# Performance work log

Measured on AMD Instinct MI355X. Metric: run time of the kernel, lower is better.

Reference implementation:

```python
import jax, jax.numpy as jnp
import numpy as np

N, C, T, V = 64, 64, 256, 25
R, O = C // 8, 64  # rel_channels, out_channels
ALPHA = 1.0


def setup_inputs() -> dict:
    key = jax.random.key(0)
    ks = jax.random.split(key, 10)
    s = 0.05
    return {
        "x": jax.random.normal(ks[0], (N, C, T, V), dtype=jnp.float32),
        "A": jax.random.normal(ks[1], (V, V), dtype=jnp.float32),
        "w1": jax.random.normal(ks[2], (R, C), dtype=jnp.float32) * s,
        "b1": jnp.zeros((R,), dtype=jnp.float32),
        "w2": jax.random.normal(ks[3], (R, C), dtype=jnp.float32) * s,
        "b2": jnp.zeros((R,), dtype=jnp.float32),
        "w3": jax.random.normal(ks[4], (O, C), dtype=jnp.float32) * s,
        "b3": jnp.zeros((O,), dtype=jnp.float32),
        "w4": jax.random.normal(ks[5], (O, R), dtype=jnp.float32) * s,
        "b4": jnp.zeros((O,), dtype=jnp.float32),
    }


def reference(x, A, w1, b1, w2, b2, w3, b3, w4, b4):
    # x: (N, C, T, V)
    # conv1/conv2 are 1x1 convs followed by mean over T -> (N, R, V)
    x1 = jnp.einsum('nctv,rc->nrv', x, w1) / x.shape[2] + b1[:, None]
    x2 = jnp.einsum('nctv,rc->nrv', x, w2) / x.shape[2] + b2[:, None]
    # conv3: 1x1 conv -> (N, O, T, V)
    x3 = jnp.einsum('nctv,oc->notv', x, w3) + b3[:, None, None]
    # outer-difference attention over joints: (N, R, V, V)
    att = jnp.tanh(x1[:, :, :, None] - x2[:, :, None, :])
    # conv4 channel mix (R->O), scale, add adjacency: (N, O, V, V)
    m = jnp.einsum('nruv,or->nouv', att, w4) + b4[:, None, None]
    m = m * ALPHA + A[None, None, :, :]
    # aggregation: einsum('ncuv,nctv->nctu')
    out = jnp.einsum('ncuv,nctv->nctu', m, x3)
    return out
```

## Files before the change

kernel.cpp:

```cpp
#include <hip/hip_runtime.h>

#define NN 64
#define CC 64
#define TT 256
#define VV 25
#define RR 8
#define OO 64
#define PLANE 6400

__global__ __launch_bounds__(256) void k_xsum(const float* __restrict__ x,
                                              float* __restrict__ xsum) {
  int nc = blockIdx.x;
  const float* src = x + (size_t)nc * PLANE;
  __shared__ float s[PLANE];
  int tid = threadIdx.x;
#pragma unroll
  for (int k = 0; k < 25; ++k) s[k * 256 + tid] = src[k * 256 + tid];
  __syncthreads();
  if (tid < VV) {
    float a0 = 0.f, a1 = 0.f, a2 = 0.f, a3 = 0.f;
    for (int t = 0; t < TT; t += 4) {
      a0 += s[(t + 0) * VV + tid];
      a1 += s[(t + 1) * VV + tid];
      a2 += s[(t + 2) * VV + tid];
      a3 += s[(t + 3) * VV + tid];
    }
    xsum[nc * VV + tid] = (a0 + a1) + (a2 + a3);
  }
}

__global__ void k_wt(const float* __restrict__ w3, float* __restrict__ w3t) {
  int k = blockIdx.x * 256 + threadIdx.x;
  if (k < 4096) {
    int c = k >> 6, o = k & 63;
    w3t[k] = w3[o * 64 + c];
  }
}

__global__ __launch_bounds__(256) void k_build_m(
    const float* __restrict__ xsum, const float* __restrict__ A,
    const float* __restrict__ w1, const float* __restrict__ b1,
    const float* __restrict__ w2, const float* __restrict__ b2,
    const float* __restrict__ w4, const float* __restrict__ b4,
    float* __restrict__ mp) {
  int n = blockIdx.x;
  __shared__ float xs[CC * VV];
  __shared__ float sx1[RR * VV];
  __shared__ float sx2[RR * VV];
  __shared__ float att[RR * 625];
  int tid = threadIdx.x;
  const float* xsn = xsum + n * (CC * VV);
  for (int k = tid; k < CC * VV; k += 256) xs[k] = xsn[k];
  __syncthreads();
  if (tid < RR * VV) {
    int r = tid / VV, v = tid % VV;
    float a1 = 0.f, a2 = 0.f;
#pragma unroll
    for (int c = 0; c < CC; ++c) {
      float xv = xs[c * VV + v];
      a1 = fmaf(w1[r * CC + c], xv, a1);
      a2 = fmaf(w2[r * CC + c], xv, a2);
    }
    sx1[tid] = a1 * (1.f / 256.f) + b1[r];
    sx2[tid] = a2 * (1.f / 256.f) + b2[r];
  }
  __syncthreads();
  for (int k = tid; k < RR * 625; k += 256) {
    int r = k / 625, uv = k % 625;
    int u = uv / VV, v = uv % VV;
    att[k] = tanhf(sx1[r * VV + u] - sx2[r * VV + v]);
  }
  __syncthreads();
  for (int k = tid; k < OO * 625; k += 256) {
    int o = k / 625, uv = k % 625;
    int u = uv / VV, v = uv % VV;
    float a = b4[o] + A[uv];
#pragma unroll
    for (int r = 0; r < RR; ++r) a = fmaf(w4[o * RR + r], att[r * 625 + uv], a);
    mp[(((size_t)n * OO + o) * VV + u) * 32 + v] = a;
  }
}

__global__ __launch_bounds__(256) void k_conv3(const float* __restrict__ x,
                                               const float* __restrict__ w3t,
                                               const float* __restrict__ b3,
                                               float* __restrict__ x3) {
  int n = blockIdx.y;
  int p = blockIdx.x * 256 + threadIdx.x;
  const float* xn = x + (size_t)n * CC * PLANE;
  float acc[OO];
#pragma unroll
  for (int o = 0; o < OO; ++o) acc[o] = b3[o];
#pragma unroll 2
  for (int c = 0; c < CC; ++c) {
    float xv = xn[(size_t)c * PLANE + p];
    const float* w = w3t + c * OO;
#pragma unroll
    for (int o = 0; o < OO; ++o) acc[o] = fmaf(w[o], xv, acc[o]);
  }
  float* dst = x3 + (size_t)n * OO * PLANE + p;
#pragma unroll
  for (int o = 0; o < OO; ++o) dst[(size_t)o * PLANE] = acc[o];
}

__global__ __launch_bounds__(256) void k_aggr(float* __restrict__ out,
                                              const float* __restrict__ mp) {
  int no = blockIdx.x;
  float* base = out + (size_t)no * PLANE;
  __shared__ float s[PLANE];
  int tid = threadIdx.x;
#pragma unroll
  for (int k = 0; k < 25; ++k) s[k * 256 + tid] = base[k * 256 + tid];
  __syncthreads();
  const float* m = mp + (size_t)no * (VV * 32);
  float xr[VV], orow[VV];
#pragma unroll
  for (int v = 0; v < VV; ++v) xr[v] = s[tid * VV + v];
#pragma unroll
  for (int u = 0; u < VV; ++u) {
    float a = 0.f;
#pragma unroll
    for (int v = 0; v < VV; ++v) a = fmaf(m[u * 32 + v], xr[v], a);
    orow[u] = a;
  }
#pragma unroll
  for (int u = 0; u < VV; ++u) s[tid * VV + u] = orow[u];
  __syncthreads();
#pragma unroll
  for (int k = 0; k < 25; ++k) base[k * 256 + tid] = s[k * 256 + tid];
}

extern "C" void kernel_launch(void* const* d_in, const int* in_sizes, int n_in,
                              void* d_out, int out_size, void* d_ws,
                              size_t ws_size, hipStream_t stream) {
  const float* x = (const float*)d_in[0];
  const float* A = (const float*)d_in[1];
  const float* w1 = (const float*)d_in[2];
  const float* b1 = (const float*)d_in[3];
  const float* w2 = (const float*)d_in[4];
  const float* b2 = (const float*)d_in[5];
  const float* w3 = (const float*)d_in[6];
  const float* b3 = (const float*)d_in[7];
  const float* w4 = (const float*)d_in[8];
  const float* b4 = (const float*)d_in[9];
  float* out = (float*)d_out;
  float* ws = (float*)d_ws;

  float* xsum = ws;
  float* w3t = ws + 102400;
  float* mp = ws + 106496;

  k_xsum<<<NN * CC, 256, 0, stream>>>(x, xsum);
  k_wt<<<16, 256, 0, stream>>>(w3, w3t);
  k_build_m<<<NN, 256, 0, stream>>>(xsum, A, w1, b1, w2, b2, w4, b4, mp);
  k_conv3<<<dim3(PLANE / 256, NN), 256, 0, stream>>>(x, w3t, b3, out);
  k_aggr<<<NN * OO, 256, 0, stream>>>(out, mp);
}
```

Before: 305.3 us.

## Fuse conv3 and aggregation into one kernel through shared memory

Merges the 1x1 conv3 and the joint aggregation into one kernel. Each block computes x3 for 8 time steps into shared memory, applies the transposed m matrix, and writes the output once, so the intermediate x3 no longer round-trips through global memory. Also folds the w3 transpose into k_xsum to drop a launch, and splits k_build_m over four output-channel groups for more parallelism, at the cost of each group recomputing att. Only 200 of 256 threads do the conv phase, and the aggregation phase keeps 50 accumulators per thread, which raises register pressure.

```diff
diff --git a/kernel.cpp b/kernel.cpp
--- a/kernel.cpp
+++ b/kernel.cpp
@@ -7,13 +7,21 @@
 #define RR 8
 #define OO 64
 #define PLANE 6400
+#define SX 226
 
 __global__ __launch_bounds__(256) void k_xsum(const float* __restrict__ x,
-                                              float* __restrict__ xsum) {
+                                              float* __restrict__ xsum,
+                                              const float* __restrict__ w3,
+                                              float* __restrict__ w3t) {
   int nc = blockIdx.x;
+  int tid = threadIdx.x;
+  if (blockIdx.x < 16) {
+    int k = blockIdx.x * 256 + tid;
+    int c = k >> 6, o = k & 63;
+    w3t[k] = w3[o * 64 + c];
+  }
   const float* src = x + (size_t)nc * PLANE;
   __shared__ float s[PLANE];
-  int tid = threadIdx.x;
 #pragma unroll
   for (int k = 0; k < 25; ++k) s[k * 256 + tid] = src[k * 256 + tid];
   __syncthreads();
@@ -29,14 +37,6 @@
   }
 }
 
-__global__ void k_wt(const float* __restrict__ w3, float* __restrict__ w3t) {
-  int k = blockIdx.x * 256 + threadIdx.x;
-  if (k < 4096) {
-    int c = k >> 6, o = k & 63;
-    w3t[k] = w3[o * 64 + c];
-  }
-}
-
 __global__ __launch_bounds__(256) void k_build_m(
     const float* __restrict__ xsum, const float* __restrict__ A,
     const float* __restrict__ w1, const float* __restrict__ b1,
@@ -44,6 +44,7 @@
     const float* __restrict__ w4, const float* __restrict__ b4,
     float* __restrict__ mp) {
   int n = blockIdx.x;
+  int og = blockIdx.y;
   __shared__ float xs[CC * VV];
   __shared__ float sx1[RR * VV];
   __shared__ float sx2[RR * VV];
@@ -71,63 +72,80 @@
     att[k] = tanhf(sx1[r * VV + u] - sx2[r * VV + v]);
   }
   __syncthreads();
-  for (int k = tid; k < OO * 625; k += 256) {
-    int o = k / 625, uv = k % 625;
-    int u = uv / VV, v = uv % VV;
-    float a = b4[o] + A[uv];
+  for (int k = tid; k < 16 * 625; k += 256) {
+    int o = og * 16 + k / 625, vu = k % 625;
+    int v = vu / VV, u = vu % VV;
+    float a = b4[o] + A[u * VV + v];
 #pragma unroll
-    for (int r = 0; r < RR; ++r) a = fmaf(w4[o * RR + r], att[r * 625 + uv], a);
-    mp[(((size_t)n * OO + o) * VV + u) * 32 + v] = a;
+    for (int r = 0; r < RR; ++r)
+      a = fmaf(w4[o * RR + r], att[r * 625 + u * VV + v], a);
+    mp[(((size_t)n * OO + o) * VV + v) * 32 + u] = a;
   }
 }
 
-__global__ __launch_bounds__(256) void k_conv3(const float* __restrict__ x,
-                                               const float* __restrict__ w3t,
-                                               const float* __restrict__ b3,
-                                               float* __restrict__ x3) {
+__global__ __launch_bounds__(256, 2) void k_fused(
+    const float* __restrict__ x, const float* __restrict__ w3t,
+    const float* __restrict__ b3, const float* __restrict__ mp,
+    float* __restrict__ out) {
   int n = blockIdx.y;
-  int p = blockIdx.x * 256 + threadIdx.x;
-  const float* xn = x + (size_t)n * CC * PLANE;
-  float acc[OO];
+  int t0 = blockIdx.x * 8;
+  __shared__ float s[OO * SX];
+  int tid = threadIdx.x;
+
+  if (tid < 200) {
+    const float* xp = x + (size_t)n * CC * PLANE + t0 * VV + tid;
+    float acc[OO];
 #pragma unroll
-  for (int o = 0; o < OO; ++o) acc[o] = b3[o];
+    for (int o = 0; o < OO; ++o) acc[o] = b3[o];
 #pragma unroll 2
-  for (int c = 0; c < CC; ++c) {
-    float xv = xn[(size_t)c * PLANE + p];
-    const float* w = w3t + c * OO;
+    for (int c = 0; c < CC; ++c) {
+      float xv = xp[(size_t)c * PLANE];
+      const float* w = w3t + c * OO;
 #pragma unroll
-    for (int o = 0; o < OO; ++o) acc[o] = fmaf(w[o], xv, acc[o]);
+      for (int o = 0; o < OO; ++o) acc[o] = fmaf(w[o], xv, acc[o]);
+    }
+#pragma unroll
+    for (int o = 0; o < OO; ++o) s[o * SX + tid] = acc[o];
   }
-  float* dst = x3 + (size_t)n * OO * PLANE + p;
+  __syncthreads();
+
+  {
+    int o = tid >> 2, tq = tid & 3;
+    const float* xA = s + o * SX + tq * VV;
+    const float* xB = xA + 4 * VV;
+    const float* mb = mp + (size_t)(n * OO + o) * VV * 32;
+    float accA[VV], accB[VV];
 #pragma unroll
-  for (int o = 0; o < OO; ++o) dst[(size_t)o * PLANE] = acc[o];
-}
+    for (int u = 0; u < VV; ++u) {
+      accA[u] = 0.f;
+      accB[u] = 0.f;
+    }
+#pragma unroll 2
+    for (int v = 0; v < VV; ++v) {
+      float xa = xA[v];
+      float xb = xB[v];
+      const float* mr = mb + v * 32;
+#pragma unroll
+      for (int u = 0; u < VV; ++u) {
+        float mv = mr[u];
+        accA[u] = fmaf(mv, xa, accA[u]);
+        accB[u] = fmaf(mv, xb, accB[u]);
+      }
+    }
+    __syncthreads();
+#pragma unroll
+    for (int u = 0; u < VV; ++u) {
+      s[o * SX + tq * VV + u] = accA[u];
+      s[o * SX + (tq + 4) * VV + u] = accB[u];
+    }
+  }
+  __syncthreads();
 
-__global__ __launch_bounds__(256) void k_aggr(float* __restrict__ out,
-                                              const float* __restrict__ mp) {
-  int no = blockIdx.x;
-  float* base = out + (size_t)no * PLANE;
-  __shared__ float s[PLANE];
-  int tid = threadIdx.x;
-#pragma unroll
-  for (int k = 0; k < 25; ++k) s[k * 256 + tid] = base[k * 256 + tid];
-  __syncthreads();
-  const float* m = mp + (size_t)no * (VV * 32);
-  float xr[VV], orow[VV];
-#pragma unroll
-  for (int v = 0; v < VV; ++v) xr[v] = s[tid * VV + v];
-#pragma unroll
-  for (int u = 0; u < VV; ++u) {
-    float a = 0.f;
-#pragma unroll
-    for (int v = 0; v < VV; ++v) a = fmaf(m[u * 32 + v], xr[v], a);
-    orow[u] = a;
+  float* ob = out + (size_t)n * OO * PLANE + t0 * VV;
+  for (int k = tid; k < OO * 200; k += 256) {
+    int oo = k / 200, p = k - oo * 200;
+    ob[(size_t)oo * PLANE + p] = s[oo * SX + p];
   }
-#pragma unroll
-  for (int u = 0; u < VV; ++u) s[tid * VV + u] = orow[u];
-  __syncthreads();
-#pragma unroll
-  for (int k = 0; k < 25; ++k) base[k * 256 + tid] = s[k * 256 + tid];
 }
 
 extern "C" void kernel_launch(void* const* d_in, const int* in_sizes, int n_in,
@@ -150,9 +168,8 @@
   float* w3t = ws + 102400;
   float* mp = ws + 106496;
 
-  k_xsum<<<NN * CC, 256, 0, stream>>>(x, xsum);
-  k_wt<<<16, 256, 0, stream>>>(w3, w3t);
-  k_build_m<<<NN, 256, 0, stream>>>(xsum, A, w1, b1, w2, b2, w4, b4, mp);
-  k_conv3<<<dim3(PLANE / 256, NN), 256, 0, stream>>>(x, w3t, b3, out);
-  k_aggr<<<NN * OO, 256, 0, stream>>>(out, mp);
+  k_xsum<<<NN * CC, 256, 0, stream>>>(x, xsum, w3, w3t);
+  k_build_m<<<dim3(NN, 4), 256, 0, stream>>>(xsum, A, w1, b1, w2, b2, w4, b4,
+                                             mp);
+  k_fused<<<dim3(TT / 8, NN), 256, 0, stream>>>(x, w3t, b3, mp, out);
 }
```

Measured after the change: 323.4 us. +5.9%, slower.
